# Performance work log

Hardware: AMD Instinct MI355X
Metric: run time of the kernel (lower is better)

The kernel has to match this reference:

```python
import jax, jax.numpy as jnp
import numpy as np

NORM_RADIUS = 5.0
SPATIAL_SCALE = 1.0
USE_DISKS = False
INVALID_FILL = 1e6


def setup_inputs() -> dict:
    key = jax.random.key(0)
    k1, k2, k3 = jax.random.split(key, 3)
    B, C, H, W = 8, 3, 512, 512
    P2 = 48  # 2 groups (pos/neg) x 24 clicks each
    x = jax.random.normal(k1, (B, C, H, W), dtype=jnp.float32)
    xy = jax.random.uniform(k2, (B, P2, 2), dtype=jnp.float32, minval=0.0, maxval=512.0)
    valid = jax.random.uniform(k3, (B, P2, 1)) < 0.9
    xy = jnp.where(valid, xy, -1.0)
    coords = jnp.concatenate([xy, jnp.zeros((B, P2, 1), jnp.float32)], axis=2)
    return {"x": x, "coords": coords}


def reference(x, coords):
    rows, cols = x.shape[2], x.shape[3]
    B, P2, _ = coords.shape
    P = P2 // 2  # clicks per group
    pts = coords[..., :2].reshape(-1, 2)              # [N, 2] (row, col), N = B*P2
    invalid = jnp.max(pts, axis=1) < 0                # flagged before scaling (as in torch)
    pts = pts * SPATIAL_SCALE
    rr = jnp.arange(rows, dtype=jnp.float32)[:, None]  # [rows, 1]
    cc = jnp.arange(cols, dtype=jnp.float32)[None, :]  # [1, cols]
    scale = NORM_RADIUS * SPATIAL_SCALE
    dr = rr[None, :, :] - pts[:, 0][:, None, None]     # [N, rows, cols]
    dc = cc[None, :, :] - pts[:, 1][:, None, None]
    if not USE_DISKS:
        dr = dr / scale
        dc = dc / scale
    d2 = dr * dr + dc * dc                             # squared distance map per point
    d2 = jnp.where(invalid[:, None, None], INVALID_FILL, d2)
    d2 = d2.reshape(B * 2, P, rows, cols).min(axis=1)  # min over clicks in each group
    if USE_DISKS:
        out = (d2 <= scale ** 2).astype(jnp.float32)
    else:
        out = jnp.tanh(2.0 * jnp.sqrt(d2))
    return out.reshape(B, 2, rows, cols)
```

## Files before the change

kernel.cpp:

```cpp
#include <hip/hip_runtime.h>

#define HH 512
#define WW 512
#define PP 24
#define NPT 48

__global__ __launch_bounds__(256) void DistMaps_37434934952233_kernel(
    const float* __restrict__ coords, float* __restrict__ out)
{
    const int blk  = blockIdx.x;
    const int map  = blk >> 8;
    const int row0 = (blk & 255) << 1;
    const int b    = map >> 1;
    const int g    = map & 1;

    constexpr float INV_SCALE = 1.0f / 5.0f;

    __shared__ float spr[PP];
    __shared__ float spc[PP];

    const int t = threadIdx.x;
    if (t < PP) {
        const float* cp = coords + (size_t)(b * NPT + g * PP + t) * 3;
        float pr = cp[0];
        float pc = cp[1];
        bool invalid = fmaxf(pr, pc) < 0.0f;
        spr[t] = invalid ? 1.0e5f : pr * INV_SCALE;
        spc[t] = invalid ? 1.0e5f : pc * INV_SCALE;
    }
    __syncthreads();

    const int r  = row0 + (t >> 7);
    const int c0 = (t & 127) << 2;

    const float rs  = (float)r  * INV_SCALE;
    const float cs0 = (float)c0 * INV_SCALE;
    const float cs1 = cs0 + INV_SCALE;
    const float cs2 = cs0 + 2.0f * INV_SCALE;
    const float cs3 = cs0 + 3.0f * INV_SCALE;

    float m0 = 1e30f, m1 = 1e30f, m2 = 1e30f, m3 = 1e30f;

    #pragma unroll
    for (int p = 0; p < PP; ++p) {
        const float pr = spr[p];
        const float pc = spc[p];
        const float dr  = rs - pr;
        const float dr2 = dr * dr;
        float d;
        d = cs0 - pc; m0 = fminf(m0, fmaf(d, d, dr2));
        d = cs1 - pc; m1 = fminf(m1, fmaf(d, d, dr2));
        d = cs2 - pc; m2 = fminf(m2, fmaf(d, d, dr2));
        d = cs3 - pc; m3 = fminf(m3, fmaf(d, d, dr2));
    }

    float4 o;
    o.x = tanhf(2.0f * sqrtf(m0));
    o.y = tanhf(2.0f * sqrtf(m1));
    o.z = tanhf(2.0f * sqrtf(m2));
    o.w = tanhf(2.0f * sqrtf(m3));

    const size_t idx = ((size_t)map * HH + r) * WW + c0;
    *reinterpret_cast<float4*>(out + idx) = o;
}

extern "C" void kernel_launch(void* const* d_in, const int* in_sizes, int n_in,
                              void* d_out, int out_size, void* d_ws, size_t ws_size,
                              hipStream_t stream) {
    (void)in_sizes; (void)n_in; (void)d_ws; (void)ws_size; (void)out_size;
    const float* coords = (const float*)d_in[1];
    float* out = (float*)d_out;
    DistMaps_37434934952233_kernel<<<4096, 256, 0, stream>>>(coords, out);
}
```

Before: 81.06 us.

## Cull far clicks per 16x64 tile and use fast exp-based tanh

Each block now covers a 16x64 pixel tile instead of two full rows. Before the main loop it keeps only the valid clicks within 16 pixels of the tile, collecting them in shared memory through an atomic counter. Tiles with no nearby click write 1.0 directly. The per-pixel tanh(sqrt) is replaced by a sqrt/exp/fast-divide formula. Together these cut the distance loop and the costly transcendental work, in exchange for a small approximation near the cutoff and a variable-length loop.

```diff
diff --git a/kernel.cpp b/kernel.cpp
--- a/kernel.cpp
+++ b/kernel.cpp
@@ -4,63 +4,85 @@
 #define WW 512
 #define PP 24
 #define NPT 48
+#define TH 16
+#define TW 64
+#define RCUT2 256.0f
+
+__device__ __forceinline__ float tanh2sqrt(float m) {
+    float s = __builtin_amdgcn_sqrtf(m);
+    float e = __expf(-4.0f * s);
+    return __fdividef(1.0f - e, 1.0f + e);
+}
 
 __global__ __launch_bounds__(256) void DistMaps_37434934952233_kernel(
     const float* __restrict__ coords, float* __restrict__ out)
 {
     const int blk  = blockIdx.x;
     const int map  = blk >> 8;
-    const int row0 = (blk & 255) << 1;
+    const int tile = blk & 255;
+    const int r0   = (tile >> 3) << 4;
+    const int c0   = (tile & 7) << 6;
     const int b    = map >> 1;
     const int g    = map & 1;
 
     constexpr float INV_SCALE = 1.0f / 5.0f;
 
-    __shared__ float spr[PP];
-    __shared__ float spc[PP];
+    __shared__ float npr[PP];
+    __shared__ float npc[PP];
+    __shared__ int   nnear;
 
     const int t = threadIdx.x;
+    if (t == 0) nnear = 0;
+    __syncthreads();
+
     if (t < PP) {
         const float* cp = coords + (size_t)(b * NPT + g * PP + t) * 3;
-        float pr = cp[0];
-        float pc = cp[1];
-        bool invalid = fmaxf(pr, pc) < 0.0f;
-        spr[t] = invalid ? 1.0e5f : pr * INV_SCALE;
-        spc[t] = invalid ? 1.0e5f : pc * INV_SCALE;
+        const float pr = cp[0];
+        const float pc = cp[1];
+        const bool valid = fmaxf(pr, pc) >= 0.0f;
+        const float dr = fmaxf(0.0f, fmaxf((float)r0 - pr, pr - (float)(r0 + TH - 1)));
+        const float dc = fmaxf(0.0f, fmaxf((float)c0 - pc, pc - (float)(c0 + TW - 1)));
+        if (valid && (dr * dr + dc * dc) <= RCUT2) {
+            const int i = atomicAdd(&nnear, 1);
+            npr[i] = pr * INV_SCALE;
+            npc[i] = pc * INV_SCALE;
+        }
     }
     __syncthreads();
 
-    const int r  = row0 + (t >> 7);
-    const int c0 = (t & 127) << 2;
+    const int r  = r0 + (t >> 4);
+    const int cc = c0 + ((t & 15) << 2);
+    const int n  = nnear;
 
-    const float rs  = (float)r  * INV_SCALE;
-    const float cs0 = (float)c0 * INV_SCALE;
-    const float cs1 = cs0 + INV_SCALE;
-    const float cs2 = cs0 + 2.0f * INV_SCALE;
-    const float cs3 = cs0 + 3.0f * INV_SCALE;
+    float4 o;
+    if (n == 0) {
+        o.x = 1.0f; o.y = 1.0f; o.z = 1.0f; o.w = 1.0f;
+    } else {
+        const float rs  = (float)r  * INV_SCALE;
+        const float cs0 = (float)cc * INV_SCALE;
+        const float cs1 = cs0 + INV_SCALE;
+        const float cs2 = cs0 + 2.0f * INV_SCALE;
+        const float cs3 = cs0 + 3.0f * INV_SCALE;
 
-    float m0 = 1e30f, m1 = 1e30f, m2 = 1e30f, m3 = 1e30f;
-
-    #pragma unroll
-    for (int p = 0; p < PP; ++p) {
-        const float pr = spr[p];
-        const float pc = spc[p];
-        const float dr  = rs - pr;
-        const float dr2 = dr * dr;
-        float d;
-        d = cs0 - pc; m0 = fminf(m0, fmaf(d, d, dr2));
-        d = cs1 - pc; m1 = fminf(m1, fmaf(d, d, dr2));
-        d = cs2 - pc; m2 = fminf(m2, fmaf(d, d, dr2));
-        d = cs3 - pc; m3 = fminf(m3, fmaf(d, d, dr2));
+        float m0 = 1e30f, m1 = 1e30f, m2 = 1e30f, m3 = 1e30f;
+        for (int p = 0; p < n; ++p) {
+            const float pr = npr[p];
+            const float pc = npc[p];
+            const float dr  = rs - pr;
+            const float dr2 = dr * dr;
+            float d;
+            d = cs0 - pc; m0 = fminf(m0, fmaf(d, d, dr2));
+            d = cs1 - pc; m1 = fminf(m1, fmaf(d, d, dr2));
+            d = cs2 - pc; m2 = fminf(m2, fmaf(d, d, dr2));
+            d = cs3 - pc; m3 = fminf(m3, fmaf(d, d, dr2));
+        }
+        o.x = tanh2sqrt(m0);
+        o.y = tanh2sqrt(m1);
+        o.z = tanh2sqrt(m2);
+        o.w = tanh2sqrt(m3);
     }
 
-    float4 o;
-    o.x = tanhf(2.0f * sqrtf(m0));
-    o.y = tanhf(2.0f * sqrtf(m1));
-    o.z = tanhf(2.0f * sqrtf(m2));
-    o.w = tanhf(2.0f * sqrtf(m3));
-
-    const size_t idx = ((size_t)map * HH + r) * WW + c0;
+    const size_t idx = ((size_t)map * HH + r) * WW + cc;
     *reinterpret_cast<float4*>(out + idx) = o;
 }
 
@@ -70,5 +92,5 @@
     (void)in_sizes; (void)n_in; (void)d_ws; (void)ws_size; (void)out_size;
     const float* coords = (const float*)d_in[1];
     float* out = (float*)d_out;
-    DistMaps_37434934952233_kernel<<<4096, 256, 0, stream>>>(coords, out);
+    DistMaps_37434934952233_kernel<<<16 * 256, 256, 0, stream>>>(coords, out);
 }
```

Result: faster. 73.34 us (-9.5%).
